# Kernel optimization log

Measured on AMD Instinct MI355X. Metric: run time of the kernel, lower is better.

Reference implementation:

```python
import jax, jax.numpy as jnp
import numpy as np

D_STATE = 16
D_CONV = 4

def layernorm(x, g, b, eps=1e-5):
    m = jnp.mean(x, -1, keepdims=True)
    v = jnp.var(x, -1, keepdims=True)
    return (x - m) / jnp.sqrt(v + eps) * g + b

def conv1x1(x, w):  # x [b,h,w,cin], w [cin,cout]
    return jnp.einsum('bhwc,cd->bhwd', x, w)

def dwconv3x3(x, w):  # x [b,h,w,C], w [3,3,1,C] (HWIO, groups=C)
    return jax.lax.conv_general_dilated(x, w, (1, 1), 'SAME',
        dimension_numbers=('NHWC', 'HWIO', 'NHWC'),
        feature_group_count=x.shape[-1])

def causal_dwconv1d(x, w, b):  # x [B,L,D], w [K,1,D]; causal depthwise conv (Mamba d_conv=4)
    xp = jnp.pad(x, ((0, 0), (D_CONV - 1, 0), (0, 0)))
    y = jax.lax.conv_general_dilated(xp, w, (1,), 'VALID',
        dimension_numbers=('NWC', 'WIO', 'NWC'),
        feature_group_count=x.shape[-1])
    return y + b

def selective_scan(deltaA, deltaBx, C):
    # deltaA, deltaBx: [B,L,D,S]; C: [B,L,S] -> y: [B,L,D]
    def step(h, inp):
        dA, dBx, c = inp
        h = dA * h + dBx
        return h, jnp.einsum('bds,bs->bd', h, c)
    h0 = jnp.zeros(deltaA.shape[:1] + deltaA.shape[2:], deltaA.dtype)
    _, ys = jax.lax.scan(step, h0,
        (jnp.swapaxes(deltaA, 0, 1), jnp.swapaxes(deltaBx, 0, 1), jnp.swapaxes(C, 0, 1)))
    return jnp.swapaxes(ys, 0, 1)

def spa_ssm(x, in_w, conv_w, conv_b, xproj_w, dt_w, dt_b, Alog, D, out_w):
    # Mamba (slow path) applied to flattened spatial sequence; x: [b,h,w,c]
    b, h, w, c = x.shape
    L = h * w
    xs = x.reshape(b, L, c)
    di = Alog.shape[0]
    xz = xs @ in_w                       # [b,L,2*di]
    xi, z = xz[..., :di], xz[..., di:]
    xi = jax.nn.silu(causal_dwconv1d(xi, conv_w, conv_b))
    dbc = xi @ xproj_w                   # [b,L,dt_rank+2*S]
    dtr = dt_w.shape[0]
    dt = jax.nn.softplus(dbc[..., :dtr] @ dt_w + dt_b)   # [b,L,di]
    B = dbc[..., dtr:dtr + D_STATE]
    C = dbc[..., dtr + D_STATE:]
    A = -jnp.exp(Alog)                   # [di,S]
    deltaA = jnp.exp(dt[..., None] * A)                  # [b,L,di,S]
    deltaBx = (dt * xi)[..., None] * B[:, :, None, :]    # [b,L,di,S]
    y = selective_scan(deltaA, deltaBx, C) + D * xi
    y = y * jax.nn.silu(z)
    return (y @ out_w).reshape(b, h, w, c)

def camba_forward(x, ln1_g, ln1_b, vin_w1, vin_dw, vin_w2, vout_dw1, vout_dw2,
                  ssm_in_w, ssm_conv_w, ssm_conv_b, ssm_xproj_w, ssm_dt_w, ssm_dt_b,
                  ssm_Alog, ssm_D, ssm_out_w, ln2_g, ln2_b, ff_w1, ff_dw, ff_w2):
    x = jnp.transpose(x, (0, 2, 3, 1))   # [b,h,w,c]
    # ESSM: v_in_head = LN -> 1x1 -> dw3x3 -> GELU -> 1x1
    x0 = conv1x1(layernorm(x, ln1_g, ln1_b), vin_w1)
    x0 = jax.nn.gelu(dwconv3x3(x0, vin_dw), approximate=False)
    x0 = conv1x1(x0, vin_w2)
    y = spa_ssm(x0, ssm_in_w, ssm_conv_w, ssm_conv_b, ssm_xproj_w,
                ssm_dt_w, ssm_dt_b, ssm_Alog, ssm_D, ssm_out_w) + x0
    # v_out_head = dw3x3 -> GELU -> dw3x3, residual
    y = dwconv3x3(jax.nn.gelu(dwconv3x3(y, vout_dw1), approximate=False), vout_dw2) + y
    x = y + x                            # block residual
    # PreNorm FeedForward (mult=4): 1x1 -> LReLU -> dw3x3 -> LReLU -> 1x1
    t = layernorm(x, ln2_g, ln2_b)
    t = jax.nn.leaky_relu(conv1x1(t, ff_w1), 0.2)
    t = jax.nn.leaky_relu(dwconv3x3(t, ff_dw), 0.2)
    t = conv1x1(t, ff_w2)
    x = t + x
    return jnp.transpose(x, (0, 3, 1, 2))

def setup_inputs() -> dict:
    key = jax.random.key(0)
    ks = jax.random.split(key, 16)
    b, c, h, w = 8, 64, 64, 64
    di, ds, dtr = 128, 16, 4
    s = 0.05
    n = lambda k, shp: jax.random.normal(k, shp, jnp.float32) * s
    dt0 = jnp.exp(jax.random.uniform(ks[1], (di,)) * (np.log(0.1) - np.log(1e-3)) + np.log(1e-3))
    return dict(
        x=jax.random.normal(ks[0], (b, c, h, w), jnp.float32),
        ln1_g=jnp.ones(c), ln1_b=jnp.zeros(c),
        vin_w1=n(ks[2], (c, c)), vin_dw=n(ks[3], (3, 3, 1, c)), vin_w2=n(ks[4], (c, c)),
        vout_dw1=n(ks[5], (3, 3, 1, c)), vout_dw2=n(ks[6], (3, 3, 1, c)),
        ssm_in_w=n(ks[7], (c, 2 * di)),
        ssm_conv_w=n(ks[8], (D_CONV, 1, di)), ssm_conv_b=jnp.zeros(di),
        ssm_xproj_w=n(ks[9], (di, dtr + 2 * ds)),
        ssm_dt_w=n(ks[10], (dtr, di)), ssm_dt_b=jnp.log(jnp.expm1(dt0)),
        ssm_Alog=jnp.log(jnp.broadcast_to(jnp.arange(1., ds + 1), (di, ds))),
        ssm_D=jnp.ones(di),
        ssm_out_w=n(ks[11], (di, c)),
        ln2_g=jnp.ones(c), ln2_b=jnp.zeros(c),
        ff_w1=n(ks[12], (c, 4 * c)), ff_dw=n(ks[13], (3, 3, 1, 4 * c)), ff_w2=n(ks[14], (4 * c, c)),
    )

def reference(x, ln1_g, ln1_b, vin_w1, vin_dw, vin_w2, vout_dw1, vout_dw2,
              ssm_in_w, ssm_conv_w, ssm_conv_b, ssm_xproj_w, ssm_dt_w, ssm_dt_b,
              ssm_Alog, ssm_D, ssm_out_w, ln2_g, ln2_b, ff_w1, ff_dw, ff_w2):
    return camba_forward(x, ln1_g, ln1_b, vin_w1, vin_dw, vin_w2, vout_dw1, vout_dw2,
                         ssm_in_w, ssm_conv_w, ssm_conv_b, ssm_xproj_w, ssm_dt_w, ssm_dt_b,
                         ssm_Alog, ssm_D, ssm_out_w, ln2_g, ln2_b, ff_w1, ff_dw, ff_w2)
```

## Files before the change

### kernel.cpp

```cpp
#include <hip/hip_runtime.h>
#include <hip/hip_bf16.h>
#include <math.h>

typedef unsigned short u16;
typedef __attribute__((ext_vector_type(8))) short s8v;
typedef __attribute__((ext_vector_type(4))) float f4v;

#define B_    8
#define C_    64
#define HW_   4096
#define NPIX  32768
#define DI    128
#define NCH   256
#define CHL   16

__device__ __forceinline__ float b2f(u16 v){ return __uint_as_float(((unsigned)v)<<16); }
__device__ __forceinline__ u16 f2b(float x){
  unsigned u = __float_as_uint(x);
  u += 0x7fff + ((u >> 16) & 1);
  return (u16)(u >> 16);
}
__device__ __forceinline__ float gelu_exact(float x){ return 0.5f*x*(1.0f+erff(x*0.70710678118654752f)); }
__device__ __forceinline__ float leaky02(float x){ return x>0.f ? x : 0.2f*x; }
__device__ __forceinline__ float softplus_(float x){ return fmaxf(x,0.f)+log1pf(__expf(-fabsf(x))); }
__device__ __forceinline__ float silu_(float x){ return x / (1.0f + __expf(-x)); }
__device__ __forceinline__ void unpack16(uint4 q0, uint4 q1, float* v){
  unsigned w[8]={q0.x,q0.y,q0.z,q0.w,q1.x,q1.y,q1.z,q1.w};
  #pragma unroll
  for(int j=0;j<8;j++){
    v[2*j]   = __uint_as_float(w[j]<<16);
    v[2*j+1] = __uint_as_float(w[j]&0xffff0000u);
  }
}

__global__ void k_prep(const float* __restrict__ vin_w1, const float* __restrict__ vin_w2,
                       const float* __restrict__ ssm_in_w, const float* __restrict__ xproj,
                       const float* __restrict__ dtw, const float* __restrict__ ssm_outw,
                       const float* __restrict__ ff_w1, const float* __restrict__ ff_w2,
                       u16* __restrict__ wv1, u16* __restrict__ wv2, u16* __restrict__ wsi,
                       u16* __restrict__ wdb, u16* __restrict__ wout, u16* __restrict__ wf1,
                       u16* __restrict__ wf2t){
  int g = blockIdx.x*256 + threadIdx.x;
  if(g < 4096){
    int n=g>>6, c=g&63;
    wv1[n*64+c]=f2b(vin_w1[c*64+n]);
    wv2[n*64+c]=f2b(vin_w2[c*64+n]);
  }
  if(g < 16384){
    int n=g>>6, c=g&63;
    wsi[n*64+c]=f2b(ssm_in_w[c*256+n]);
    wf1[n*64+c]=f2b(ff_w1[c*256+n]);
    int n2=g/256, k2=g%256;
    wf2t[n2*256+k2]=f2b(ff_w2[k2*64+n2]);
  }
  if(g < 8192){
    int n=g>>7, k=g&127;
    wout[n*128+k]=f2b(ssm_outw[k*64+n]);
  }
  if(g < 20480){
    int n=g/128, k=g%128;
    float v;
    if(n < 128){
      v = 0.f;
      for(int r=0;r<4;r++) v += xproj[k*36+r]*dtw[r*128+n];
    }else{
      v = xproj[k*36+4+(n-128)];
    }
    wdb[n*128+k]=f2b(v);
  }
}

__global__ __launch_bounds__(256) void k_trans_ln_mm(const float* __restrict__ x,
                     const float* __restrict__ g, const float* __restrict__ bta,
                     const u16* __restrict__ wT,
                     u16* __restrict__ xT, u16* __restrict__ outp){
  const int LDA = 72, NS = 4;
  __shared__ float tile[64][65];
  __shared__ __align__(16) u16 sA[64*LDA];
  __shared__ __align__(16) u16 sW[64*LDA];
  int tid = threadIdx.x;
  int blk = blockIdx.x;
  int b = blk >> 6;
  int hwb = (blk & 63) << 6;
  int lane = tid & 63, row = tid >> 6;
  const float* src = x + (size_t)b*C_*HW_;
  #pragma unroll
  for(int k=0;k<16;k++){
    int c = row + 4*k;
    tile[c][lane] = src[c*HW_ + hwb + lane];
  }
  for(int idx=tid; idx<64*8; idx+=256){
    int n = idx>>3, c8 = (idx&7)*8;
    *(uint4*)(sW + n*LDA + c8) = *(const uint4*)(wT + n*64 + c8);
  }
  __syncthreads();
  u16* dstT = xT + (size_t)b*HW_*C_;
  #pragma unroll
  for(int k=0;k<16;k++){
    int hwl = row + 4*k;
    dstT[(hwb+hwl)*C_ + lane] = f2b(tile[lane][hwl]);
  }
  float gg = g[lane], bb = bta[lane];
  #pragma unroll
  for(int i=0;i<16;i++){
    int hwl = row*16 + i;
    float v = tile[lane][hwl];
    float s = v, sq = v*v;
    #pragma unroll
    for(int o=32;o>0;o>>=1){ s += __shfl_xor(s,o); sq += __shfl_xor(sq,o); }
    float m = s*(1.f/64.f);
    float var = sq*(1.f/64.f) - m*m;
    float r = rsqrtf(var + 1e-5f);
    sA[hwl*LDA + lane] = f2b((v-m)*r*gg + bb);
  }
  __syncthreads();
  int ln = tid & 63, wv = tid >> 6;
  int mrow = ln & 15, quad = ln >> 4;
  f4v acc[NS];
  #pragma unroll
  for(int i=0;i<NS;i++) acc[i] = (f4v){0.f,0.f,0.f,0.f};
  const u16* aBase = sA + (wv*16 + mrow)*LDA + quad*8;
  const u16* wBase = sW + mrow*LDA + quad*8;
  #pragma unroll
  for(int kk=0; kk<64; kk+=32){
    s8v af = *(const s8v*)(aBase + kk);
    #pragma unroll
    for(int ns=0; ns<NS; ns++){
      s8v bf = *(const s8v*)(wBase + ns*16*LDA + kk);
      acc[ns] = __builtin_amdgcn_mfma_f32_16x16x32_bf16(af, bf, acc[ns], 0, 0, 0);
    }
  }
  int p0 = blk*64;
  int pr = p0 + wv*16 + quad*4;
  #pragma unroll
  for(int ns=0; ns<NS; ns++){
    int n = ns*16 + mrow;
    #pragma unroll
    for(int r=0;r<4;r++)
      outp[(size_t)(pr+r)*64 + n] = f2b(acc[ns][r]);
  }
}

__global__ __launch_bounds__(256) void k_dw3mm(const u16* __restrict__ in,
                     const float* __restrict__ dwgt, const u16* __restrict__ wT,
                     u16* __restrict__ x0){
  const int LDT = 72;
  __shared__ __align__(16) u16 sIn[10*10*64];
  __shared__ __align__(16) u16 sT[64*LDT];
  __shared__ __align__(16) u16 sW[64*LDT];
  int tid = threadIdx.x;
  int blk = blockIdx.x;
  int b = blk >> 6;
  int t6 = blk & 63;
  int h0 = (t6 >> 3) * 8, w0 = (t6 & 7) * 8;
  for(int idx=tid; idx<64*8; idx+=256){
    int n = idx>>3, c8 = (idx&7)*8;
    *(uint4*)(sW + n*LDT + c8) = *(const uint4*)(wT + n*64 + c8);
  }
  for(int q=tid; q<10*10*16; q+=256){
    int pp = q >> 4, c4 = q & 15;
    int hh = pp / 10, ww = pp % 10;
    int gh = h0-1+hh, gw = w0-1+ww;
    ushort4 v = make_ushort4(0,0,0,0);
    if((unsigned)gh < 64u && (unsigned)gw < 64u)
      v = *(const ushort4*)(in + (size_t)((b*64+gh)*64+gw)*64 + c4*4);
    *(ushort4*)(sIn + pp*64 + c4*4) = v;
  }
  __syncthreads();
  int c4 = tid & 15;
  #pragma unroll
  for(int pass=0; pass<4; pass++){
    int opix = pass*16 + (tid>>4);
    int oh = opix >> 3, ow = opix & 7;
    float a0=0.f,a1=0.f,a2=0.f,a3=0.f;
    #pragma unroll
    for(int kh=0;kh<3;kh++){
      #pragma unroll
      for(int kw=0;kw<3;kw++){
        ushort4 v = *(const ushort4*)(sIn + ((oh+kh)*10 + (ow+kw))*64 + c4*4);
        float4 wv = *(const float4*)(dwgt + (kh*3+kw)*64 + c4*4);
        a0 += b2f(v.x)*wv.x; a1 += b2f(v.y)*wv.y;
        a2 += b2f(v.z)*wv.z; a3 += b2f(v.w)*wv.w;
      }
    }
    ushort4 o; o.x=f2b(gelu_exact(a0)); o.y=f2b(gelu_exact(a1));
    o.z=f2b(gelu_exact(a2)); o.w=f2b(gelu_exact(a3));
    *(ushort4*)(sT + opix*LDT + c4*4) = o;
  }
  __syncthreads();
  int ln = tid & 63, wv = tid >> 6;
  int mrow = ln & 15, quad = ln >> 4;
  f4v acc[4];
  #pragma unroll
  for(int i=0;i<4;i++) acc[i] = (f4v){0.f,0.f,0.f,0.f};
  const u16* aBase = sT + (wv*16 + mrow)*LDT + quad*8;
  const u16* wBase = sW + mrow*LDT + quad*8;
  #pragma unroll
  for(int kk=0; kk<64; kk+=32){
    s8v af = *(const s8v*)(aBase + kk);
    #pragma unroll
    for(int ns=0; ns<4; ns++){
      s8v bf = *(const s8v*)(wBase + ns*16*LDT + kk);
      acc[ns] = __builtin_amdgcn_mfma_f32_16x16x32_bf16(af, bf, acc[ns], 0, 0, 0);
    }
  }
  #pragma unroll
  for(int ns=0; ns<4; ns++){
    int n = ns*16 + mrow;
    #pragma unroll
    for(int r=0;r<4;r++){
      int opix = wv*16 + quad*4 + r;
      int oh = opix >> 3, ow = opix & 7;
      size_t p = ((size_t)(b*64 + h0+oh)*64 + (w0+ow));
      x0[p*64 + n] = f2b(acc[ns][r]);
    }
  }
}

__global__ __launch_bounds__(256) void k_ssm_dtbc(const u16* __restrict__ wT,
                     const u16* __restrict__ x0,
                     const float* __restrict__ cw, const float* __restrict__ cb,
                     const u16* __restrict__ wdb, const float* __restrict__ dtbias,
                     u16* __restrict__ xi, u16* __restrict__ zs,
                     u16* __restrict__ dtout, u16* __restrict__ bcout){
  const int LDA=72, NS=16, LDY=136, LDWD=136, NS2=10;
  __shared__ __align__(16) u16 S[31616];
  u16* sW   = S;
  u16* sA   = S + 18432;
  u16* ubuf = S + 23040;
  u16* xiT  = S;
  u16* wdbS = S + 8704;
  int tid = threadIdx.x;
  int p0 = blockIdx.x*64;
  int ln = tid & 63, wv = tid >> 6;
  int mrow = ln & 15, quad = ln >> 4;
  for(int idx=tid; idx<256*8; idx+=256){
    int n = idx>>3, c8 = (idx&7)*8;
    *(uint4*)(sW + n*LDA + c8) = *(const uint4*)(wT + n*64 + c8);
  }
  for(int g=tid; g<64*8; g+=256){
    int row = g >> 3, c8 = (g & 7)*8;
    *(uint4*)(sA + row*LDA + c8) = *(const uint4*)(x0 + (size_t)(p0+row)*64 + c8);
  }
  __syncthreads();
  f4v acc[NS];
  #pragma unroll
  for(int i=0;i<NS;i++) acc[i] = (f4v){0.f,0.f,0.f,0.f};
  const u16* aBase = sA + (wv*16 + mrow)*LDA + quad*8;
  const u16* wBase = sW + mrow*LDA + quad*8;
  #pragma unroll
  for(int kk=0; kk<64; kk+=32){
    s8v af = *(const s8v*)(aBase + kk);
    #pragma unroll
    for(int ns=0; ns<NS; ns++){
      s8v bf = *(const s8v*)(wBase + ns*16*LDA + kk);
      acc[ns] = __builtin_amdgcn_mfma_f32_16x16x32_bf16(af, bf, acc[ns], 0, 0, 0);
    }
  }
  bool bstart = ((p0 & 4095) == 0);
  for(int idx=tid; idx<384; idx+=256){
    int j = idx >> 7, n = idx & 127;
    float a2 = 0.f;
    if(!bstart){
      const u16* xr = x0 + (size_t)(p0-3+j)*64;
      #pragma unroll 8
      for(int c=0;c<64;c++) a2 += b2f(xr[c]) * b2f(sW[n*LDA+c]);
    }
    ubuf[j*128 + n] = f2b(a2);
  }
  int prl = wv*16 + quad*4;
  #pragma unroll
  for(int ns=0; ns<NS; ns++){
    int n = ns*16 + mrow;
    if(n < 128){
      #pragma unroll
      for(int r=0;r<4;r++) ubuf[(prl+r+3)*128 + n] = f2b(acc[ns][r]);
    }else{
      #pragma unroll
      for(int r=0;r<4;r++) zs[(size_t)(p0+prl+r)*128 + (n-128)] = f2b(silu_(acc[ns][r]));
    }
  }
  __syncthreads();
  int d4 = tid & 31;
  float4 cbv = *(const float4*)(cb + d4*4);
  for(int row = tid >> 5; row < 64; row += 8){
    float a0=cbv.x, a1=cbv.y, a2=cbv.z, a3=cbv.w;
    #pragma unroll
    for(int k=0;k<4;k++){
      ushort4 v = *(const ushort4*)(ubuf + (row+k)*128 + d4*4);
      float4 wv4 = *(const float4*)(cw + k*128 + d4*4);
      a0 += b2f(v.x)*wv4.x; a1 += b2f(v.y)*wv4.y;
      a2 += b2f(v.z)*wv4.z; a3 += b2f(v.w)*wv4.w;
    }
    ushort4 o; o.x=f2b(silu_(a0)); o.y=f2b(silu_(a1)); o.z=f2b(silu_(a2)); o.w=f2b(silu_(a3));
    *(ushort4*)(xi + (size_t)(p0+row)*128 + d4*4) = o;
    *(ushort4*)(xiT + row*LDY + d4*4) = o;
  }
  __syncthreads();
  for(int idx=tid; idx<160*16; idx+=256){
    int n = idx>>4, c8 = (idx&15)*8;
    *(uint4*)(wdbS + n*LDWD + c8) = *(const uint4*)(wdb + n*128 + c8);
  }
  __syncthreads();
  f4v acc2[NS2];
  #pragma unroll
  for(int i=0;i<NS2;i++) acc2[i] = (f4v){0.f,0.f,0.f,0.f};
  #pragma unroll
  for(int kk=0; kk<128; kk+=32){
    s8v af = *(const s8v*)(xiT + (wv*16+mrow)*LDY + kk + quad*8);
    #pragma unroll
    for(int ns=0; ns<NS2; ns++){
      s8v bf = *(const s8v*)(wdbS + (ns*16+mrow)*LDWD + kk + quad*8);
      acc2[ns] = __builtin_amdgcn_mfma_f32_16x16x32_bf16(af, bf, acc2[ns], 0, 0, 0);
    }
  }
  int pr = p0 + wv*16 + quad*4;
  #pragma unroll
  for(int ns=0; ns<NS2; ns++){
    int n = ns*16 + mrow;
    if(n < 128){
      float bs = dtbias[n];
      #pragma unroll
      for(int r=0;r<4;r++)
        dtout[(size_t)(pr+r)*128 + n] = f2b(softplus_(acc2[ns][r] + bs));
    }else{
      #pragma unroll
      for(int r=0;r<4;r++)
        bcout[(size_t)(pr+r)*32 + (n-128)] = f2b(acc2[ns][r]);
    }
  }
}

__global__ __launch_bounds__(256) void k_scan1(const u16* __restrict__ dt, const u16* __restrict__ xi,
                        const u16* __restrict__ bc, const float* __restrict__ alog,
                        u16* __restrict__ Pb, u16* __restrict__ Qb){
  int t = blockIdx.x*256 + threadIdx.x;
  int d = t & 127;
  int ch = (t >> 7) & 255;
  int b = t >> 15;
  int pbase = b*HW_ + ch*CHL;
  float A[16];
  #pragma unroll
  for(int s=0;s<16;s++) A[s] = -__expf(alog[d*16+s]);
  float dtv[16], uv[16];
  #pragma unroll
  for(int i=0;i<CHL;i++){
    dtv[i] = b2f(dt[(size_t)(pbase+i)*128 + d]);
    uv[i]  = dtv[i] * b2f(xi[(size_t)(pbase+i)*128 + d]);
  }
  float Q[16], sumdt = 0.f;
  #pragma unroll
  for(int s=0;s<16;s++) Q[s] = 0.f;
  #pragma unroll
  for(int i=0;i<CHL;i++){
    float Bv[16];
    unpack16(*(const uint4*)(bc + (size_t)(pbase+i)*32),
             *(const uint4*)(bc + (size_t)(pbase+i)*32 + 8), Bv);
    sumdt += dtv[i];
    #pragma unroll
    for(int s=0;s<16;s++){
      float a = __expf(dtv[i]*A[s]);
      Q[s] = a*Q[s] + uv[i]*Bv[s];
    }
  }
  int gidx = ch*16384 + (b*128+d)*16;
  unsigned pw[8], qw[8];
  #pragma unroll
  for(int j=0;j<8;j++){
    pw[j] = (unsigned)f2b(__expf(A[2*j]*sumdt)) | ((unsigned)f2b(__expf(A[2*j+1]*sumdt))<<16);
    qw[j] = (unsigned)f2b(Q[2*j]) | ((unsigned)f2b(Q[2*j+1])<<16);
  }
  *(uint4*)(Pb+gidx)   = make_uint4(pw[0],pw[1],pw[2],pw[3]);
  *(uint4*)(Pb+gidx+8) = make_uint4(pw[4],pw[5],pw[6],pw[7]);
  *(uint4*)(Qb+gidx)   = make_uint4(qw[0],qw[1],qw[2],qw[3]);
  *(uint4*)(Qb+gidx+8) = make_uint4(qw[4],qw[5],qw[6],qw[7]);
}

__global__ __launch_bounds__(256) void k_scan2(const u16* __restrict__ Pb, const u16* __restrict__ Qb,
                        u16* __restrict__ Hin){
  __shared__ __align__(16) u16 sP[256*32];
  __shared__ __align__(16) u16 sQ[256*32];
  __shared__ float gP[8*32];
  __shared__ float gQ[8*32];
  int tid = threadIdx.x;
  int s0 = blockIdx.x * 32;
  for(int idx = tid; idx < 256*4; idx += 256){
    int ch = idx >> 2, j8 = (idx & 3) * 8;
    *(uint4*)(sP + ch*32 + j8) = *(const uint4*)(Pb + (size_t)ch*16384 + s0 + j8);
    *(uint4*)(sQ + ch*32 + j8) = *(const uint4*)(Qb + (size_t)ch*16384 + s0 + j8);
  }
  __syncthreads();
  int sl = tid & 31, grp = tid >> 5;
  int base = grp * 32;
  float P = 1.f, Q = 0.f;
  #pragma unroll 8
  for(int c = 0; c < 32; c++){
    float p = b2f(sP[(base+c)*32 + sl]);
    float q = b2f(sQ[(base+c)*32 + sl]);
    P = p * P;
    Q = p * Q + q;
  }
  gP[grp*32 + sl] = P;
  gQ[grp*32 + sl] = Q;
  __syncthreads();
  float h = 0.f;
  #pragma unroll
  for(int g = 0; g < 7; g++){
    if(g < grp) h = gP[g*32 + sl] * h + gQ[g*32 + sl];
  }
  for(int c = 0; c < 32; c++){
    Hin[(size_t)(base+c)*16384 + s0 + sl] = f2b(h);
    float p = b2f(sP[(base+c)*32 + sl]);
    float q = b2f(sQ[(base+c)*32 + sl]);
    h = p * h + q;
  }
}

__global__ __launch_bounds__(128) void k_scan3_mm(const u16* __restrict__ dt, const u16* __restrict__ xi,
                        const u16* __restrict__ bc, const u16* __restrict__ zs,
                        const float* __restrict__ alog, const float* __restrict__ Dp,
                        const u16* __restrict__ Hin, const u16* __restrict__ wout,
                        const u16* __restrict__ x0, u16* __restrict__ y){
  const int LDY = 136, LDW = 136;
  int blk = blockIdx.x;
  int ch = blk & (NCH-1);
  int b = blk >> 8;
  int d = threadIdx.x, tid = threadIdx.x;
  __shared__ __align__(16) u16 sY[CHL*LDY];
  __shared__ __align__(16) u16 sWo[64*LDW];
  __shared__ __align__(16) u16 sbc[CHL*32];
  for(int idx=tid; idx<64*16; idx+=128){
    int n = idx>>4, c8 = (idx&15)*8;
    *(uint4*)(sWo + n*LDW + c8) = *(const uint4*)(wout + n*128 + c8);
  }
  int pbase = b*HW_ + ch*CHL;
  if(tid < 64) ((uint4*)sbc)[tid] = ((const uint4*)(bc + (size_t)pbase*32))[tid];
  float A[16], h[16];
  u16 hbuf[16];
  int gidx = ch*16384 + (b*128+d)*16;
  *(uint4*)hbuf     = *(const uint4*)(Hin+gidx);
  *(uint4*)(hbuf+8) = *(const uint4*)(Hin+gidx+8);
  #pragma unroll
  for(int s=0;s<16;s++){ A[s] = -__expf(alog[d*16+s]); h[s] = b2f(hbuf[s]); }
  float Dd = Dp[d];
  float dtv[16], xiv[16], zsv[16];
  #pragma unroll
  for(int i=0;i<CHL;i++){
    dtv[i] = b2f(dt[(size_t)(pbase+i)*128 + d]);
    xiv[i] = b2f(xi[(size_t)(pbase+i)*128 + d]);
    zsv[i] = b2f(zs[(size_t)(pbase+i)*128 + d]);
  }
  __syncthreads();
  #pragma unroll
  for(int i=0;i<CHL;i++){
    float Bv[16], Cv[16];
    unpack16(*(const uint4*)(sbc + i*32),      *(const uint4*)(sbc + i*32 + 8),  Bv);
    unpack16(*(const uint4*)(sbc + i*32 + 16), *(const uint4*)(sbc + i*32 + 24), Cv);
    float u = dtv[i]*xiv[i];
    float acc = Dd*xiv[i];
    #pragma unroll
    for(int s=0;s<16;s++){
      float a = __expf(dtv[i]*A[s]);
      h[s] = a*h[s] + u*Bv[s];
      acc += h[s]*Cv[s];
    }
    sY[i*LDY + d] = f2b(acc * zsv[i]);
  }
  __syncthreads();
  int ln = tid & 63, wv = tid >> 6;
  int mrow = ln & 15, quad = ln >> 4;
  f4v acc2[2];
  acc2[0] = (f4v){0.f,0.f,0.f,0.f};
  acc2[1] = (f4v){0.f,0.f,0.f,0.f};
  #pragma unroll
  for(int kk=0; kk<128; kk+=32){
    s8v af = *(const s8v*)(sY + mrow*LDY + kk + quad*8);
    #pragma unroll
    for(int ns=0; ns<2; ns++){
      int n0 = wv*32 + ns*16;
      s8v bf = *(const s8v*)(sWo + (n0+mrow)*LDW + kk + quad*8);
      acc2[ns] = __builtin_amdgcn_mfma_f32_16x16x32_bf16(af, bf, acc2[ns], 0, 0, 0);
    }
  }
  #pragma unroll
  for(int ns=0; ns<2; ns++){
    int n = wv*32 + ns*16 + mrow;
    #pragma unroll
    for(int r=0;r<4;r++){
      int px = pbase + quad*4 + r;
      y[(size_t)px*64 + n] = f2b(acc2[ns][r] + b2f(x0[(size_t)px*64 + n]));
    }
  }
}

__global__ __launch_bounds__(256) void k_dw3x2(const u16* __restrict__ yin,
                      const float* __restrict__ w1, const float* __restrict__ w2,
                      const u16* __restrict__ xTr, u16* __restrict__ outp){
  const int LDH = 68;
  __shared__ __align__(16) u16 sY[144*LDH];
  __shared__ __align__(16) u16 sT[100*LDH];
  int tid = threadIdx.x;
  int blk = blockIdx.x;
  int b = blk >> 6;
  int t6 = blk & 63;
  int h0 = (t6 >> 3) * 8, w0 = (t6 & 7) * 8;
  for(int q=tid; q<144*16; q+=256){
    int pp = q >> 4, c4 = q & 15;
    int hh = pp / 12, ww = pp - hh*12;
    int gh = h0-2+hh, gw = w0-2+ww;
    ushort4 v = make_ushort4(0,0,0,0);
    if((unsigned)gh < 64u && (unsigned)gw < 64u)
      v = *(const ushort4*)(yin + (size_t)((b*64+gh)*64+gw)*64 + c4*4);
    *(ushort4*)(sY + pp*LDH + c4*4) = v;
  }
  __syncthreads();
  int c4 = tid & 15;
  #pragma unroll
  for(int pass=0; pass<7; pass++){
    int tpix = pass*16 + (tid>>4);
    if(tpix < 100){
      int th = tpix / 10, tw = tpix - th*10;
      int gh = h0-1+th, gw = w0-1+tw;
      ushort4 o = make_ushort4(0,0,0,0);
      if((unsigned)gh < 64u && (unsigned)gw < 64u){
        float a0=0.f,a1=0.f,a2=0.f,a3=0.f;
        #pragma unroll
        for(int kh=0;kh<3;kh++){
          #pragma unroll
          for(int kw=0;kw<3;kw++){
            ushort4 v = *(const ushort4*)(sY + ((th+kh)*12 + (tw+kw))*LDH + c4*4);
            float4 wv = *(const float4*)(w1 + (kh*3+kw)*64 + c4*4);
            a0 += b2f(v.x)*wv.x; a1 += b2f(v.y)*wv.y;
            a2 += b2f(v.z)*wv.z; a3 += b2f(v.w)*wv.w;
          }
        }
        o.x=f2b(gelu_exact(a0)); o.y=f2b(gelu_exact(a1));
        o.z=f2b(gelu_exact(a2)); o.w=f2b(gelu_exact(a3));
      }
      *(ushort4*)(sT + tpix*LDH + c4*4) = o;
    }
  }
  __syncthreads();
  #pragma unroll
  for(int pass=0; pass<4; pass++){
    int opix = pass*16 + (tid>>4);
    int oh = opix >> 3, ow = opix & 7;
    float a0=0.f,a1=0.f,a2=0.f,a3=0.f;
    #pragma unroll
    for(int kh=0;kh<3;kh++){
      #pragma unroll
      for(int kw=0;kw<3;kw++){
        ushort4 v = *(const ushort4*)(sT + ((oh+kh)*10 + (ow+kw))*LDH + c4*4);
        float4 wv = *(const float4*)(w2 + (kh*3+kw)*64 + c4*4);
        a0 += b2f(v.x)*wv.x; a1 += b2f(v.y)*wv.y;
        a2 += b2f(v.z)*wv.z; a3 += b2f(v.w)*wv.w;
      }
    }
    size_t gp = (size_t)((b*64 + h0+oh)*64 + (w0+ow));
    ushort4 ry = *(const ushort4*)(sY + ((oh+2)*12 + (ow+2))*LDH + c4*4);
    ushort4 rx = *(const ushort4*)(xTr + gp*64 + c4*4);
    a0 += b2f(ry.x); a0 += b2f(rx.x);
    a1 += b2f(ry.y); a1 += b2f(rx.y);
    a2 += b2f(ry.z); a2 += b2f(rx.z);
    a3 += b2f(ry.w); a3 += b2f(rx.w);
    ushort4 o; o.x=f2b(a0); o.y=f2b(a1); o.z=f2b(a2); o.w=f2b(a3);
    *(ushort4*)(outp + gp*64 + c4*4) = o;
  }
}

__global__ __launch_bounds__(256) void k_ffn(const u16* __restrict__ xR,
                     const float* __restrict__ g, const float* __restrict__ bta,
                     const u16* __restrict__ wf1, const u16* __restrict__ wf2t,
                     const float* __restrict__ fdw, float* __restrict__ outp){
  const int LDX = 72;
  __shared__ __align__(16) u16 sX[112*LDX];
  __shared__ __align__(16) u16 sT1[112*LDX];
  __shared__ __align__(16) u16 sW1[64*LDX];
  __shared__ __align__(16) u16 sW2[64*LDX];
  __shared__ float sDW[9*256];
  int tid = threadIdx.x;
  int blk = blockIdx.x;
  int b = blk >> 6;
  int t6 = blk & 63;
  int h0 = (t6 >> 3)*8, w0 = (t6 & 7)*8;
  int ln = tid & 63, wv = tid >> 6;
  int mrow = ln & 15, quad = ln >> 4;
  for(int i=tid; i<9*64; i+=256) ((float4*)sDW)[i] = ((const float4*)fdw)[i];
  float gg = g[ln], bb = bta[ln];
  for(int hp = wv; hp < 112; hp += 4){
    u16 o = 0;
    if(hp < 100){
      int th = hp/10, tw = hp - th*10;
      int gh = h0-1+th, gw = w0-1+tw;
      if((unsigned)gh < 64u && (unsigned)gw < 64u){
        float v = b2f(xR[(size_t)((b*64+gh)*64+gw)*64 + ln]);
        float s = v, sq = v*v;
        #pragma unroll
        for(int o2=32;o2>0;o2>>=1){ s += __shfl_xor(s,o2); sq += __shfl_xor(sq,o2); }
        float m = s*(1.f/64.f);
        float var = sq*(1.f/64.f) - m*m;
        float r = rsqrtf(var + 1e-5f);
        o = f2b((v-m)*r*gg + bb);
      }
    }
    sX[hp*LDX + ln] = o;
  }
  f4v acc2[4];
  #pragma unroll
  for(int i=0;i<4;i++) acc2[i] = (f4v){0.f,0.f,0.f,0.f};
  int p = wv*16 + mrow;
  int oh = p >> 3, ow = p & 7;
  for(int c=0; c<4; c++){
    int nc0 = c*64;
    __syncthreads();
    for(int idx=tid; idx<64*8; idx+=256){
      int n = idx>>3, c8 = (idx&7)*8;
      *(uint4*)(sW1 + n*LDX + c8) = *(const uint4*)(wf1 + (size_t)(nc0+n)*64 + c8);
      *(uint4*)(sW2 + n*LDX + c8) = *(const uint4*)(wf2t + (size_t)n*256 + nc0 + c8);
    }
    __syncthreads();
    for(int mt = wv; mt < 7; mt += 4){
      f4v a1[4];
      #pragma unroll
      for(int i=0;i<4;i++) a1[i] = (f4v){0.f,0.f,0.f,0.f};
      const u16* aB = sX + (mt*16 + mrow)*LDX + quad*8;
      const u16* wB = sW1 + mrow*LDX + quad*8;
      #pragma unroll
      for(int kk=0; kk<64; kk+=32){
        s8v af = *(const s8v*)(aB + kk);
        #pragma unroll
        for(int ns=0; ns<4; ns++){
          s8v bf = *(const s8v*)(wB + ns*16*LDX + kk);
          a1[ns] = __builtin_amdgcn_mfma_f32_16x16x32_bf16(af, bf, a1[ns], 0, 0, 0);
        }
      }
      #pragma unroll
      for(int ns=0; ns<4; ns++)
        #pragma unroll
        for(int r=0; r<4; r++)
          sT1[(mt*16 + quad*4 + r)*LDX + ns*16 + mrow] = f2b(leaky02(a1[ns][r]));
    }
    __syncthreads();
    #pragma unroll
    for(int half=0; half<2; half++){
      int ch0 = half*32 + quad*8;
      float a[8];
      #pragma unroll
      for(int j=0;j<8;j++) a[j] = 0.f;
      #pragma unroll
      for(int kh=0;kh<3;kh++){
        #pragma unroll
        for(int kw=0;kw<3;kw++){
          s8v v = *(const s8v*)(sT1 + ((oh+kh)*10 + (ow+kw))*LDX + ch0);
          const float* wp = sDW + (kh*3+kw)*256 + nc0 + ch0;
          float4 w0v = *(const float4*)(wp);
          float4 w1v = *(const float4*)(wp+4);
          a[0] += b2f((u16)v[0])*w0v.x; a[1] += b2f((u16)v[1])*w0v.y;
          a[2] += b2f((u16)v[2])*w0v.z; a[3] += b2f((u16)v[3])*w0v.w;
          a[4] += b2f((u16)v[4])*w1v.x; a[5] += b2f((u16)v[5])*w1v.y;
          a[6] += b2f((u16)v[6])*w1v.z; a[7] += b2f((u16)v[7])*w1v.w;
        }
      }
      s8v af;
      #pragma unroll
      for(int j=0;j<8;j++) af[j] = (short)f2b(leaky02(a[j]));
      #pragma unroll
      for(int ns=0; ns<4; ns++){
        s8v bf = *(const s8v*)(sW2 + (ns*16 + mrow)*LDX + half*32 + quad*8);
        acc2[ns] = __builtin_amdgcn_mfma_f32_16x16x32_bf16(af, bf, acc2[ns], 0, 0, 0);
      }
    }
  }
  int pe = wv*16 + quad*4;
  int eoh = pe >> 3, eow0 = pe & 7;
  size_t gbase = (size_t)((b*64 + h0 + eoh)*64 + (w0 + eow0));
  #pragma unroll
  for(int ns=0; ns<4; ns++){
    int n = ns*16 + mrow;
    float4 v4;
    v4.x = acc2[ns][0] + b2f(xR[(gbase+0)*64 + n]);
    v4.y = acc2[ns][1] + b2f(xR[(gbase+1)*64 + n]);
    v4.z = acc2[ns][2] + b2f(xR[(gbase+2)*64 + n]);
    v4.w = acc2[ns][3] + b2f(xR[(gbase+3)*64 + n]);
    *(float4*)(outp + (size_t)b*C_*HW_ + (size_t)n*HW_ + (h0+eoh)*64 + (w0+eow0)) = v4;
  }
}

extern "C" void kernel_launch(void* const* d_in, const int* in_sizes, int n_in,
                              void* d_out, int out_size, void* d_ws, size_t ws_size,
                              hipStream_t stream) {
  const float* x        = (const float*)d_in[0];
  const float* ln1_g    = (const float*)d_in[1];
  const float* ln1_b    = (const float*)d_in[2];
  const float* vin_w1   = (const float*)d_in[3];
  const float* vin_dw   = (const float*)d_in[4];
  const float* vin_w2   = (const float*)d_in[5];
  const float* vout_dw1 = (const float*)d_in[6];
  const float* vout_dw2 = (const float*)d_in[7];
  const float* ssm_in_w = (const float*)d_in[8];
  const float* ssm_cw   = (const float*)d_in[9];
  const float* ssm_cb   = (const float*)d_in[10];
  const float* ssm_xprj = (const float*)d_in[11];
  const float* ssm_dtw  = (const float*)d_in[12];
  const float* ssm_dtb  = (const float*)d_in[13];
  const float* ssm_Alog = (const float*)d_in[14];
  const float* ssm_D    = (const float*)d_in[15];
  const float* ssm_outw = (const float*)d_in[16];
  const float* ln2_g    = (const float*)d_in[17];
  const float* ln2_b    = (const float*)d_in[18];
  const float* ff_w1    = (const float*)d_in[19];
  const float* ff_dw    = (const float*)d_in[20];
  const float* ff_w2    = (const float*)d_in[21];
  float* out = (float*)d_out;

  const size_t M = 1u<<20;
  u16* U   = (u16*)d_ws;
  u16* xT  = U;
  u16* tA  = U + 2*M;
  u16* tB  = U + 4*M;
  u16* x0  = U + 6*M;
  u16* xi  = U + 8*M;
  u16* zs  = U + 12*M;
  u16* dtb = U + 24*M;
  u16* bc  = U + 28*M;
  u16* Pb  = U + 16*M;
  u16* Qb  = U + 20*M;
  u16* Hin = tA;
  u16* y   = U + 16*M;
  u16* wv1  = U + 33*M;
  u16* wv2  = wv1 + 4096;
  u16* wsi  = wv2 + 4096;
  u16* wdb  = wsi + 16384;
  u16* wout = wdb + 20480;
  u16* wf1  = wout + 8192;
  u16* wf2t = wf1 + 16384;

  k_prep<<<80,256,0,stream>>>(vin_w1, vin_w2, ssm_in_w, ssm_xprj, ssm_dtw, ssm_outw,
                              ff_w1, ff_w2, wv1, wv2, wsi, wdb, wout, wf1, wf2t);

  k_trans_ln_mm<<<512,256,0,stream>>>(x, ln1_g, ln1_b, wv1, xT, tB);
  k_dw3mm<<<512,256,0,stream>>>(tB, vin_dw, wv2, x0);

  k_ssm_dtbc<<<512,256,0,stream>>>(wsi, x0, ssm_cw, ssm_cb, wdb, ssm_dtb,
                                   xi, zs, dtb, bc);
  k_scan1<<<1024,256,0,stream>>>(dtb, xi, bc, ssm_Alog, Pb, Qb);
  k_scan2<<<512,256,0,stream>>>(Pb, Qb, Hin);
  k_scan3_mm<<<2048,128,0,stream>>>(dtb, xi, bc, zs, ssm_Alog, ssm_D, Hin, wout, x0, y);

  k_dw3x2<<<512,256,0,stream>>>(y, vout_dw1, vout_dw2, xT, x0);

  k_ffn<<<512,256,0,stream>>>(x0, ln2_g, ln2_b, wf1, wf2t, ff_dw, out);
}
```

Baseline: 247.1 us.

## Fuse chunk scan pass into dtbc kernel and vout depthwise convs into FFN

The first-pass chunk scan (P/Q computation) now runs at the end of k_ssm_dtbc. It reads dt, xi and B from shared memory already in the block instead of reloading them from global memory, which removes one launch. The two vout depthwise 3x3 convolutions plus residuals are folded into the FFN kernel, using a 14x14 halo tile and dynamic shared memory. That skips writing and rereading the intermediate x0 tensor. In exchange the FFN blocks redo halo work, use much more LDS (which may lower occupancy), and the scan work runs with fewer threads per block.

```diff
diff --git a/kernel.cpp b/kernel.cpp
--- a/kernel.cpp
+++ b/kernel.cpp
@@ -221,15 +221,19 @@
                      const u16* __restrict__ x0,
                      const float* __restrict__ cw, const float* __restrict__ cb,
                      const u16* __restrict__ wdb, const float* __restrict__ dtbias,
+                     const float* __restrict__ alog,
                      u16* __restrict__ xi, u16* __restrict__ zs,
-                     u16* __restrict__ dtout, u16* __restrict__ bcout){
-  const int LDA=72, NS=16, LDY=136, LDWD=136, NS2=10;
+                     u16* __restrict__ dtout, u16* __restrict__ bcout,
+                     u16* __restrict__ Pb, u16* __restrict__ Qb){
+  const int LDA=72, NS=16, LDY=136, LDWD=136, NS2=10, LDD=136;
   __shared__ __align__(16) u16 S[31616];
   u16* sW   = S;
   u16* sA   = S + 18432;
   u16* ubuf = S + 23040;
   u16* xiT  = S;
   u16* wdbS = S + 8704;
+  u16* sdt  = S + 8704;
+  u16* sbc2 = S + 17408;
   int tid = threadIdx.x;
   int p0 = blockIdx.x*64;
   int ln = tid & 63, wv = tid >> 6;
@@ -314,66 +318,67 @@
       acc2[ns] = __builtin_amdgcn_mfma_f32_16x16x32_bf16(af, bf, acc2[ns], 0, 0, 0);
     }
   }
-  int pr = p0 + wv*16 + quad*4;
+  __syncthreads();
+  int pr = p0 + prl;
   #pragma unroll
   for(int ns=0; ns<NS2; ns++){
     int n = ns*16 + mrow;
     if(n < 128){
       float bs = dtbias[n];
       #pragma unroll
-      for(int r=0;r<4;r++)
-        dtout[(size_t)(pr+r)*128 + n] = f2b(softplus_(acc2[ns][r] + bs));
+      for(int r=0;r<4;r++){
+        u16 dv = f2b(softplus_(acc2[ns][r] + bs));
+        dtout[(size_t)(pr+r)*128 + n] = dv;
+        sdt[(prl+r)*LDD + n] = dv;
+      }
     }else{
       #pragma unroll
-      for(int r=0;r<4;r++)
-        bcout[(size_t)(pr+r)*32 + (n-128)] = f2b(acc2[ns][r]);
-    }
-  }
-}
-
-__global__ __launch_bounds__(256) void k_scan1(const u16* __restrict__ dt, const u16* __restrict__ xi,
-                        const u16* __restrict__ bc, const float* __restrict__ alog,
-                        u16* __restrict__ Pb, u16* __restrict__ Qb){
-  int t = blockIdx.x*256 + threadIdx.x;
-  int d = t & 127;
-  int ch = (t >> 7) & 255;
-  int b = t >> 15;
-  int pbase = b*HW_ + ch*CHL;
-  float A[16];
-  #pragma unroll
-  for(int s=0;s<16;s++) A[s] = -__expf(alog[d*16+s]);
-  float dtv[16], uv[16];
-  #pragma unroll
-  for(int i=0;i<CHL;i++){
-    dtv[i] = b2f(dt[(size_t)(pbase+i)*128 + d]);
-    uv[i]  = dtv[i] * b2f(xi[(size_t)(pbase+i)*128 + d]);
-  }
-  float Q[16], sumdt = 0.f;
-  #pragma unroll
-  for(int s=0;s<16;s++) Q[s] = 0.f;
-  #pragma unroll
-  for(int i=0;i<CHL;i++){
-    float Bv[16];
-    unpack16(*(const uint4*)(bc + (size_t)(pbase+i)*32),
-             *(const uint4*)(bc + (size_t)(pbase+i)*32 + 8), Bv);
-    sumdt += dtv[i];
-    #pragma unroll
-    for(int s=0;s<16;s++){
-      float a = __expf(dtv[i]*A[s]);
-      Q[s] = a*Q[s] + uv[i]*Bv[s];
-    }
-  }
-  int gidx = ch*16384 + (b*128+d)*16;
-  unsigned pw[8], qw[8];
-  #pragma unroll
-  for(int j=0;j<8;j++){
-    pw[j] = (unsigned)f2b(__expf(A[2*j]*sumdt)) | ((unsigned)f2b(__expf(A[2*j+1]*sumdt))<<16);
-    qw[j] = (unsigned)f2b(Q[2*j]) | ((unsigned)f2b(Q[2*j+1])<<16);
-  }
-  *(uint4*)(Pb+gidx)   = make_uint4(pw[0],pw[1],pw[2],pw[3]);
-  *(uint4*)(Pb+gidx+8) = make_uint4(pw[4],pw[5],pw[6],pw[7]);
-  *(uint4*)(Qb+gidx)   = make_uint4(qw[0],qw[1],qw[2],qw[3]);
-  *(uint4*)(Qb+gidx+8) = make_uint4(qw[4],qw[5],qw[6],qw[7]);
+      for(int r=0;r<4;r++){
+        u16 bv = f2b(acc2[ns][r]);
+        bcout[(size_t)(pr+r)*32 + (n-128)] = bv;
+        sbc2[(prl+r)*36 + (n-128)] = bv;
+      }
+    }
+  }
+  __syncthreads();
+  {
+    int d = tid & 127;
+    int cp = tid >> 7;
+    float A[16];
+    #pragma unroll
+    for(int s=0;s<16;s++) A[s] = -__expf(alog[d*16+s]);
+    int bI = p0 >> 12;
+    int chbase = (p0 & 4095) >> 4;
+    for(int cc = 2*cp; cc < 2*cp+2; cc++){
+      int r0 = cc*16;
+      float Q[16], sumdt = 0.f;
+      #pragma unroll
+      for(int s=0;s<16;s++) Q[s] = 0.f;
+      #pragma unroll
+      for(int i=0;i<CHL;i++){
+        float dtv = b2f(sdt[(r0+i)*LDD + d]);
+        float uv  = dtv * b2f(xiT[(r0+i)*LDY + d]);
+        sumdt += dtv;
+        #pragma unroll
+        for(int s=0;s<16;s++){
+          float Bv = b2f(sbc2[(r0+i)*36 + s]);
+          float a = __expf(dtv*A[s]);
+          Q[s] = a*Q[s] + uv*Bv;
+        }
+      }
+      int gidx = (chbase+cc)*16384 + (bI*128+d)*16;
+      unsigned pw[8], qw[8];
+      #pragma unroll
+      for(int j=0;j<8;j++){
+        pw[j] = (unsigned)f2b(__expf(A[2*j]*sumdt)) | ((unsigned)f2b(__expf(A[2*j+1]*sumdt))<<16);
+        qw[j] = (unsigned)f2b(Q[2*j]) | ((unsigned)f2b(Q[2*j+1])<<16);
+      }
+      *(uint4*)(Pb+gidx)   = make_uint4(pw[0],pw[1],pw[2],pw[3]);
+      *(uint4*)(Pb+gidx+8) = make_uint4(pw[4],pw[5],pw[6],pw[7]);
+      *(uint4*)(Qb+gidx)   = make_uint4(qw[0],qw[1],qw[2],qw[3]);
+      *(uint4*)(Qb+gidx+8) = make_uint4(qw[4],qw[5],qw[6],qw[7]);
+    }
+  }
 }
 
 __global__ __launch_bounds__(256) void k_scan2(const u16* __restrict__ Pb, const u16* __restrict__ Qb,
@@ -493,91 +498,22 @@
   }
 }
 
-__global__ __launch_bounds__(256) void k_dw3x2(const u16* __restrict__ yin,
-                      const float* __restrict__ w1, const float* __restrict__ w2,
-                      const u16* __restrict__ xTr, u16* __restrict__ outp){
-  const int LDH = 68;
-  __shared__ __align__(16) u16 sY[144*LDH];
-  __shared__ __align__(16) u16 sT[100*LDH];
-  int tid = threadIdx.x;
-  int blk = blockIdx.x;
-  int b = blk >> 6;
-  int t6 = blk & 63;
-  int h0 = (t6 >> 3) * 8, w0 = (t6 & 7) * 8;
-  for(int q=tid; q<144*16; q+=256){
-    int pp = q >> 4, c4 = q & 15;
-    int hh = pp / 12, ww = pp - hh*12;
-    int gh = h0-2+hh, gw = w0-2+ww;
-    ushort4 v = make_ushort4(0,0,0,0);
-    if((unsigned)gh < 64u && (unsigned)gw < 64u)
-      v = *(const ushort4*)(yin + (size_t)((b*64+gh)*64+gw)*64 + c4*4);
-    *(ushort4*)(sY + pp*LDH + c4*4) = v;
-  }
-  __syncthreads();
-  int c4 = tid & 15;
-  #pragma unroll
-  for(int pass=0; pass<7; pass++){
-    int tpix = pass*16 + (tid>>4);
-    if(tpix < 100){
-      int th = tpix / 10, tw = tpix - th*10;
-      int gh = h0-1+th, gw = w0-1+tw;
-      ushort4 o = make_ushort4(0,0,0,0);
-      if((unsigned)gh < 64u && (unsigned)gw < 64u){
-        float a0=0.f,a1=0.f,a2=0.f,a3=0.f;
-        #pragma unroll
-        for(int kh=0;kh<3;kh++){
-          #pragma unroll
-          for(int kw=0;kw<3;kw++){
-            ushort4 v = *(const ushort4*)(sY + ((th+kh)*12 + (tw+kw))*LDH + c4*4);
-            float4 wv = *(const float4*)(w1 + (kh*3+kw)*64 + c4*4);
-            a0 += b2f(v.x)*wv.x; a1 += b2f(v.y)*wv.y;
-            a2 += b2f(v.z)*wv.z; a3 += b2f(v.w)*wv.w;
-          }
-        }
-        o.x=f2b(gelu_exact(a0)); o.y=f2b(gelu_exact(a1));
-        o.z=f2b(gelu_exact(a2)); o.w=f2b(gelu_exact(a3));
-      }
-      *(ushort4*)(sT + tpix*LDH + c4*4) = o;
-    }
-  }
-  __syncthreads();
-  #pragma unroll
-  for(int pass=0; pass<4; pass++){
-    int opix = pass*16 + (tid>>4);
-    int oh = opix >> 3, ow = opix & 7;
-    float a0=0.f,a1=0.f,a2=0.f,a3=0.f;
-    #pragma unroll
-    for(int kh=0;kh<3;kh++){
-      #pragma unroll
-      for(int kw=0;kw<3;kw++){
-        ushort4 v = *(const ushort4*)(sT + ((oh+kh)*10 + (ow+kw))*LDH + c4*4);
-        float4 wv = *(const float4*)(w2 + (kh*3+kw)*64 + c4*4);
-        a0 += b2f(v.x)*wv.x; a1 += b2f(v.y)*wv.y;
-        a2 += b2f(v.z)*wv.z; a3 += b2f(v.w)*wv.w;
-      }
-    }
-    size_t gp = (size_t)((b*64 + h0+oh)*64 + (w0+ow));
-    ushort4 ry = *(const ushort4*)(sY + ((oh+2)*12 + (ow+2))*LDH + c4*4);
-    ushort4 rx = *(const ushort4*)(xTr + gp*64 + c4*4);
-    a0 += b2f(ry.x); a0 += b2f(rx.x);
-    a1 += b2f(ry.y); a1 += b2f(rx.y);
-    a2 += b2f(ry.z); a2 += b2f(rx.z);
-    a3 += b2f(ry.w); a3 += b2f(rx.w);
-    ushort4 o; o.x=f2b(a0); o.y=f2b(a1); o.z=f2b(a2); o.w=f2b(a3);
-    *(ushort4*)(outp + gp*64 + c4*4) = o;
-  }
-}
-
-__global__ __launch_bounds__(256) void k_ffn(const u16* __restrict__ xR,
+__global__ __launch_bounds__(256) void k_ffn2(const u16* __restrict__ yin,
+                     const float* __restrict__ w1, const float* __restrict__ w2,
+                     const u16* __restrict__ xTr,
                      const float* __restrict__ g, const float* __restrict__ bta,
                      const u16* __restrict__ wf1, const u16* __restrict__ wf2t,
                      const float* __restrict__ fdw, float* __restrict__ outp){
   const int LDX = 72;
-  __shared__ __align__(16) u16 sX[112*LDX];
-  __shared__ __align__(16) u16 sT1[112*LDX];
-  __shared__ __align__(16) u16 sW1[64*LDX];
-  __shared__ __align__(16) u16 sW2[64*LDX];
-  __shared__ float sDW[9*256];
+  extern __shared__ __align__(16) u16 S[];
+  u16* sX  = S;
+  u16* sC  = S + 8064;
+  u16* sYh = S + 12672;
+  u16* sT  = S + 26784;
+  u16* sT1 = S + 12672;
+  u16* sW1 = S + 20736;
+  u16* sW2 = S + 25344;
+  float* sDW = (float*)(S + 29952);
   int tid = threadIdx.x;
   int blk = blockIdx.x;
   int b = blk >> 6;
@@ -585,6 +521,69 @@
   int h0 = (t6 >> 3)*8, w0 = (t6 & 7)*8;
   int ln = tid & 63, wv = tid >> 6;
   int mrow = ln & 15, quad = ln >> 4;
+  for(int q=tid; q<196*16; q+=256){
+    int pp = q >> 4, c4 = q & 15;
+    int hh = pp / 14, ww = pp - hh*14;
+    int gh = h0-3+hh, gw = w0-3+ww;
+    ushort4 v = make_ushort4(0,0,0,0);
+    if((unsigned)gh < 64u && (unsigned)gw < 64u)
+      v = *(const ushort4*)(yin + (size_t)((b*64+gh)*64+gw)*64 + c4*4);
+    *(ushort4*)(sYh + pp*LDX + c4*4) = v;
+  }
+  __syncthreads();
+  for(int q=tid; q<144*16; q+=256){
+    int tpix = q >> 4, c4 = q & 15;
+    int th = tpix / 12, tw = tpix - th*12;
+    int gh = h0-2+th, gw = w0-2+tw;
+    ushort4 o = make_ushort4(0,0,0,0);
+    if((unsigned)gh < 64u && (unsigned)gw < 64u){
+      float a0=0.f,a1=0.f,a2=0.f,a3=0.f;
+      #pragma unroll
+      for(int kh=0;kh<3;kh++){
+        #pragma unroll
+        for(int kw=0;kw<3;kw++){
+          ushort4 v = *(const ushort4*)(sYh + ((th+kh)*14 + (tw+kw))*LDX + c4*4);
+          float4 wv4 = *(const float4*)(w1 + (kh*3+kw)*64 + c4*4);
+          a0 += b2f(v.x)*wv4.x; a1 += b2f(v.y)*wv4.y;
+          a2 += b2f(v.z)*wv4.z; a3 += b2f(v.w)*wv4.w;
+        }
+      }
+      o.x=f2b(gelu_exact(a0)); o.y=f2b(gelu_exact(a1));
+      o.z=f2b(gelu_exact(a2)); o.w=f2b(gelu_exact(a3));
+    }
+    *(ushort4*)(sT + tpix*LDX + c4*4) = o;
+  }
+  __syncthreads();
+  for(int q=tid; q<100*16; q+=256){
+    int xpix = q >> 4, c4 = q & 15;
+    int xh = xpix / 10, xw = xpix - xh*10;
+    int gh = h0-1+xh, gw = w0-1+xw;
+    ushort4 o = make_ushort4(0,0,0,0);
+    if((unsigned)gh < 64u && (unsigned)gw < 64u){
+      float a0=0.f,a1=0.f,a2=0.f,a3=0.f;
+      #pragma unroll
+      for(int kh=0;kh<3;kh++){
+        #pragma unroll
+        for(int kw=0;kw<3;kw++){
+          ushort4 v = *(const ushort4*)(sT + ((xh+kh)*12 + (xw+kw))*LDX + c4*4);
+          float4 wv4 = *(const float4*)(w2 + (kh*3+kw)*64 + c4*4);
+          a0 += b2f(v.x)*wv4.x; a1 += b2f(v.y)*wv4.y;
+          a2 += b2f(v.z)*wv4.z; a3 += b2f(v.w)*wv4.w;
+        }
+      }
+      ushort4 ry = *(const ushort4*)(sYh + ((xh+2)*14 + (xw+2))*LDX + c4*4);
+      ushort4 rx = *(const ushort4*)(xTr + (size_t)((b*64+gh)*64+gw)*64 + c4*4);
+      a0 += b2f(ry.x) + b2f(rx.x);
+      a1 += b2f(ry.y) + b2f(rx.y);
+      a2 += b2f(ry.z) + b2f(rx.z);
+      a3 += b2f(ry.w) + b2f(rx.w);
+      o.x=f2b(a0); o.y=f2b(a1); o.z=f2b(a2); o.w=f2b(a3);
+    }
+    *(ushort4*)(sX + xpix*LDX + c4*4) = o;
+    if(xh>=1 && xh<=8 && xw>=1 && xw<=8)
+      *(ushort4*)(sC + ((xh-1)*8 + (xw-1))*LDX + c4*4) = o;
+  }
+  __syncthreads();
   for(int i=tid; i<9*64; i+=256) ((float4*)sDW)[i] = ((const float4*)fdw)[i];
   float gg = g[ln], bb = bta[ln];
   for(int hp = wv; hp < 112; hp += 4){
@@ -593,7 +592,7 @@
       int th = hp/10, tw = hp - th*10;
       int gh = h0-1+th, gw = w0-1+tw;
       if((unsigned)gh < 64u && (unsigned)gw < 64u){
-        float v = b2f(xR[(size_t)((b*64+gh)*64+gw)*64 + ln]);
+        float v = b2f(sX[hp*LDX + ln]);
         float s = v, sq = v*v;
         #pragma unroll
         for(int o2=32;o2>0;o2>>=1){ s += __shfl_xor(s,o2); sq += __shfl_xor(sq,o2); }
@@ -673,15 +672,14 @@
   }
   int pe = wv*16 + quad*4;
   int eoh = pe >> 3, eow0 = pe & 7;
-  size_t gbase = (size_t)((b*64 + h0 + eoh)*64 + (w0 + eow0));
   #pragma unroll
   for(int ns=0; ns<4; ns++){
     int n = ns*16 + mrow;
     float4 v4;
-    v4.x = acc2[ns][0] + b2f(xR[(gbase+0)*64 + n]);
-    v4.y = acc2[ns][1] + b2f(xR[(gbase+1)*64 + n]);
-    v4.z = acc2[ns][2] + b2f(xR[(gbase+2)*64 + n]);
-    v4.w = acc2[ns][3] + b2f(xR[(gbase+3)*64 + n]);
+    v4.x = acc2[ns][0] + b2f(sC[(pe+0)*LDX + n]);
+    v4.y = acc2[ns][1] + b2f(sC[(pe+1)*LDX + n]);
+    v4.z = acc2[ns][2] + b2f(sC[(pe+2)*LDX + n]);
+    v4.w = acc2[ns][3] + b2f(sC[(pe+3)*LDX + n]);
     *(float4*)(outp + (size_t)b*C_*HW_ + (size_t)n*HW_ + (h0+eoh)*64 + (w0+eow0)) = v4;
   }
 }
@@ -735,19 +733,24 @@
   u16* wf1  = wout + 8192;
   u16* wf2t = wf1 + 16384;
 
+  static bool attr_set = false;
+  if(!attr_set){
+    hipFuncSetAttribute((const void*)k_ffn2,
+                        hipFuncAttributeMaxDynamicSharedMemorySize, 74304);
+    attr_set = true;
+  }
+
   k_prep<<<80,256,0,stream>>>(vin_w1, vin_w2, ssm_in_w, ssm_xprj, ssm_dtw, ssm_outw,
                               ff_w1, ff_w2, wv1, wv2, wsi, wdb, wout, wf1, wf2t);
 
   k_trans_ln_mm<<<512,256,0,stream>>>(x, ln1_g, ln1_b, wv1, xT, tB);
   k_dw3mm<<<512,256,0,stream>>>(tB, vin_dw, wv2, x0);
 
-  k_ssm_dtbc<<<512,256,0,stream>>>(wsi, x0, ssm_cw, ssm_cb, wdb, ssm_dtb,
-                                   xi, zs, dtb, bc);
-  k_scan1<<<1024,256,0,stream>>>(dtb, xi, bc, ssm_Alog, Pb, Qb);
+  k_ssm_dtbc<<<512,256,0,stream>>>(wsi, x0, ssm_cw, ssm_cb, wdb, ssm_dtb, ssm_Alog,
+                                   xi, zs, dtb, bc, Pb, Qb);
   k_scan2<<<512,256,0,stream>>>(Pb, Qb, Hin);
   k_scan3_mm<<<2048,128,0,stream>>>(dtb, xi, bc, zs, ssm_Alog, ssm_D, Hin, wout, x0, y);
 
-  k_dw3x2<<<512,256,0,stream>>>(y, vout_dw1, vout_dw2, xT, x0);
-
-  k_ffn<<<512,256,0,stream>>>(x0, ln2_g, ln2_b, wf1, wf2t, ff_dw, out);
-}
+  k_ffn2<<<512,256,74304,stream>>>(y, vout_dw1, vout_dw2, xT, ln2_g, ln2_b,
+                                   wf1, wf2t, ff_dw, out);
+}
```

Result: slower. 258.3 us (+4.5%).
